# Optimization experiments

Measured on AMD Instinct MI355X. Metric: run time of the kernel, lower is better.

## Reference

```python
import jax, jax.numpy as jnp
import numpy as np

DIM = 192
HEADS = 6
HEAD_DIM = DIM // HEADS
K = 3          # kernel_size
PAD = 1
STRIDE = 2
SCALE = HEAD_DIM ** -0.5
B, H, W = 16, 56, 56


def setup_inputs() -> dict:
    key = jax.random.key(0)
    ks = jax.random.split(key, 6)
    x = jax.random.normal(ks[0], (B, H, W, DIM), jnp.float32)
    # Linear weights stored as [in, out] so y = x @ W + b (== torch x @ W.T)
    Wv = jax.random.normal(ks[1], (DIM, DIM), jnp.float32) * 0.05          # v_pj, no bias
    Wa = jax.random.normal(ks[2], (DIM, K**4 * HEADS), jnp.float32) * 0.05  # attn linear
    ba = jax.random.normal(ks[3], (K**4 * HEADS,), jnp.float32) * 0.01
    Wp = jax.random.normal(ks[4], (DIM, DIM), jnp.float32) * 0.05           # proj
    bp = jax.random.normal(ks[5], (DIM,), jnp.float32) * 0.01
    return {"x": x, "Wv": Wv, "Wa": Wa, "ba": ba, "Wp": Wp, "bp": bp}


def reference(x, Wv, Wa, ba, Wp, bp):
    # Dropout layers act as identity (eval mode).
    Bn, Hn, Wn, C = x.shape
    h = -(-Hn // STRIDE)  # ceil(H/stride) = 28
    w = -(-Wn // STRIDE)
    KK = K * K

    # --- value projection + unfold (im2col over K x K window, stride STRIDE) ---
    v = x @ Wv  # [B,H,W,C]
    vp = jnp.pad(v, ((0, 0), (PAD, PAD), (PAD, PAD), (0, 0)))
    # patches: [B,h,w,K*K,C]; loop is over the fixed 3x3 kernel taps only
    patches = jnp.stack(
        [vp[:, i:i + STRIDE * h:STRIDE, j:j + STRIDE * w:STRIDE, :]
         for i in range(K) for j in range(K)], axis=3)
    patches = patches.reshape(Bn, h * w, KK, HEADS, HEAD_DIM)

    # --- attention weights from avg-pooled map (H divisible by STRIDE here) ---
    pooled = x.reshape(Bn, h, STRIDE, w, STRIDE, C).mean(axis=(2, 4))  # [B,h,w,C]
    a = pooled.reshape(Bn, h * w, C) @ Wa + ba                         # [B,hw,K^4*heads]
    a = a.reshape(Bn, h * w, HEADS, KK, KK) * SCALE
    a = jax.nn.softmax(a, axis=-1)

    # --- windowed attention: [B,hw,heads,K2,K2] x [B,hw,K2,heads,hd] ---
    out = jnp.einsum('bnhpq,bnqhd->bnphd', a, patches)  # [B,hw,K2,heads,hd]
    out = out.reshape(Bn, h, w, KK, C)

    # --- fold (scatter-add of overlapping patches back to HxW) ---
    acc = jnp.zeros((Bn, Hn + 2 * PAD, Wn + 2 * PAD, C), x.dtype)
    idx = 0
    for i in range(K):
        for j in range(K):
            acc = acc.at[:, i:i + STRIDE * h:STRIDE, j:j + STRIDE * w:STRIDE, :].add(out[:, :, :, idx, :])
            idx += 1
    y = acc[:, PAD:PAD + Hn, PAD:PAD + Wn, :]

    return y @ Wp + bp
```

## Files before the change

### kernel.cpp

```cpp
#include <hip/hip_runtime.h>
#include <cstdint>
#include <cstddef>

#define DIMC    192
#define NHEADS  6
#define NATT    486
#define NB      16
#define NH      56
#define NWW     56
#define HPOOL   28
#define WPOOL   28
#define NPIX    784
#define VH      58
#define VW      58
#define MROWS   (NB*NH*NWW)
#define MPOOL   (NB*NPIX)
#define SCALE_A 0.17677669529663687f

using bf16x8 = __attribute__((ext_vector_type(8))) short;
using f32x4  = __attribute__((ext_vector_type(4))) float;

static __device__ __forceinline__ unsigned short f2bf(float f) {
    unsigned int u = __float_as_uint(f);
    unsigned int r = (u + 0x7fffu + ((u >> 16) & 1u)) >> 16;
    return (unsigned short)r;
}
static __device__ __forceinline__ float bf2f(unsigned short u) {
    return __uint_as_float((unsigned int)u << 16);
}

__global__ __launch_bounds__(256)
void prep_kernel(const float* __restrict__ Wv, const float* __restrict__ Wp,
                 const float* __restrict__ Wa,
                 unsigned short* __restrict__ WTv, unsigned short* __restrict__ WTp,
                 unsigned short* __restrict__ WaT, unsigned int* __restrict__ vpu)
{
    int idx = blockIdx.x * 256 + threadIdx.x;
    if (idx < 73728) {
        int sel = idx / 36864;
        int r   = idx - sel * 36864;
        int n   = r / DIMC;
        int k   = r - n * DIMC;
        const float* W = sel ? Wp : Wv;
        unsigned short* WT = sel ? WTp : WTv;
        WT[r] = f2bf(W[k * DIMC + n]);
    } else if (idx < 172032) {
        int r = idx - 73728;
        int n = r / DIMC;
        int k = r - n * DIMC;
        WaT[r] = (n < NATT) ? f2bf(Wa[(size_t)k * NATT + n] * SCALE_A) : (unsigned short)0;
    } else {
        int i2   = idx - 172032;
        int cu   = i2 % 96;
        int rest = i2 / 96;
        int b    = rest / 228;
        int p    = rest - b * 228;
        int hi, wi;
        if (p < 58)       { hi = 0;  wi = p; }
        else if (p < 116) { hi = 57; wi = p - 58; }
        else { int q = p - 116; hi = 1 + (q >> 1); wi = (q & 1) * 57; }
        vpu[(((size_t)b * VH + hi) * VW + wi) * 96 + cu] = 0u;
    }
}

template<int MODE>
__global__ __launch_bounds__(512)
void gemm128_kernel(const void* __restrict__ Av, const unsigned short* __restrict__ WT,
                    const float* __restrict__ bias, void* __restrict__ Cv)
{
    __shared__ unsigned short As[128 * DIMC];

    const int t  = threadIdx.x;
    const int l  = t & 63;
    const int w  = t >> 6;
    const int wr = w >> 1;
    const int wc = w & 1;
    const int by = blockIdx.x;

    if (MODE == 0) {
        const float* Ab = (const float*)Av + (size_t)by * 128 * DIMC;
#pragma unroll
        for (int i = 0; i < 12; ++i) {
            int f = i * 2048 + t * 4;
            float4 v = *(const float4*)(Ab + f);
            int row = f / DIMC;
            int k   = f - row * DIMC;
            ushort4 u;
            u.x = f2bf(v.x); u.y = f2bf(v.y); u.z = f2bf(v.z); u.w = f2bf(v.w);
            int off = (row * 384 + k * 2) ^ ((row & 7) << 4);
            *(ushort4*)((char*)As + off) = u;
        }
    } else {
        const unsigned short* Ab = (const unsigned short*)Av + (size_t)by * 128 * DIMC;
#pragma unroll
        for (int i = 0; i < 6; ++i) {
            int f = i * 4096 + t * 8;
            bf16x8 v = *(const bf16x8*)(Ab + f);
            int row = f / DIMC;
            int k   = f - row * DIMC;
            int off = (row * 384 + k * 2) ^ ((row & 7) << 4);
            *(bf16x8*)((char*)As + off) = v;
        }
    }
    __syncthreads();

    f32x4 acc[2][6];
#pragma unroll
    for (int mi = 0; mi < 2; ++mi)
#pragma unroll
        for (int ni = 0; ni < 6; ++ni) acc[mi][ni] = (f32x4)0.f;

    const int arow0 = wr * 32 + (l & 15);
    const int kb    = (l >> 4) << 4;

#pragma unroll
    for (int ks = 0; ks < 6; ++ks) {
        bf16x8 a[2], b[6];
#pragma unroll
        for (int mi = 0; mi < 2; ++mi) {
            int row = arow0 + mi * 16;
            int off = (row * 384 + ks * 64 + kb) ^ ((row & 7) << 4);
            a[mi] = *(const bf16x8*)((const char*)As + off);
        }
#pragma unroll
        for (int ni = 0; ni < 6; ++ni) {
            int n = wc * 96 + ni * 16 + (l & 15);
            b[ni] = *(const bf16x8*)(WT + (size_t)n * DIMC + ks * 32 + ((l >> 4) << 3));
        }
#pragma unroll
        for (int mi = 0; mi < 2; ++mi)
#pragma unroll
            for (int ni = 0; ni < 6; ++ni)
                acc[mi][ni] = __builtin_amdgcn_mfma_f32_16x16x32_bf16(
                    a[mi], b[ni], acc[mi][ni], 0, 0, 0);
    }

    if (MODE == 0) {
        __syncthreads();
#pragma unroll
        for (int mi = 0; mi < 2; ++mi) {
#pragma unroll
            for (int r = 0; r < 4; ++r) {
                int row = wr * 32 + mi * 16 + ((l >> 4) << 2) + r;
#pragma unroll
                for (int ni = 0; ni < 6; ++ni) {
                    int col = wc * 96 + ni * 16 + (l & 15);
                    As[row * DIMC + col] = f2bf(acc[mi][ni][r]);
                }
            }
        }
        __syncthreads();
#pragma unroll
        for (int i = 0; i < 6; ++i) {
            int f   = i * 4096 + t * 8;
            int row = f / DIMC;
            int k   = f - row * DIMC;
            int m   = by * 128 + row;
            int bb  = m / (NH * NWW);
            int rr  = m - bb * (NH * NWW);
            int hi  = rr / NWW;
            int wi  = rr - hi * NWW;
            bf16x8 v = *(const bf16x8*)&As[f];
            unsigned short* dst = (unsigned short*)Cv +
                (((size_t)bb * VH + hi + 1) * VW + (wi + 1)) * DIMC + k;
            *(bf16x8*)dst = v;
        }
    } else {
        float* fAs = (float*)As;
#pragma unroll
        for (int chunk = 0; chunk < 4; ++chunk) {
            __syncthreads();
            if (wr == chunk) {
#pragma unroll
                for (int mi = 0; mi < 2; ++mi) {
#pragma unroll
                    for (int r = 0; r < 4; ++r) {
                        int rowl = mi * 16 + ((l >> 4) << 2) + r;
#pragma unroll
                        for (int ni = 0; ni < 6; ++ni) {
                            int col = wc * 96 + ni * 16 + (l & 15);
                            fAs[rowl * DIMC + col] = acc[mi][ni][r];
                        }
                    }
                }
            }
            __syncthreads();
#pragma unroll
            for (int i = 0; i < 3; ++i) {
                int f   = i * 2048 + t * 4;
                int row = f / DIMC;
                int k   = f - row * DIMC;
                int m   = by * 128 + chunk * 32 + row;
                float4 v  = *(const float4*)&fAs[f];
                float4 bv = *(const float4*)&bias[k];
                v.x += bv.x; v.y += bv.y; v.z += bv.z; v.w += bv.w;
                *(float4*)((float*)Cv + (size_t)m * DIMC + k) = v;
            }
        }
    }
}

__global__ __launch_bounds__(512)
void pool_attn_mfma_kernel(const float* __restrict__ x, const unsigned short* __restrict__ WaT,
                           const float* __restrict__ ba, unsigned short* __restrict__ attn)
{
    __shared__ unsigned short As[64 * DIMC];
    __shared__ float Cs[16][489];
    __shared__ float ba_s[NATT];

    const int t  = threadIdx.x;
    const int l  = t & 63;
    const int w  = t >> 6;
    const int wr = w >> 2;
    const int wc = w & 3;
    const int by = blockIdx.x;

    if (t < NATT) ba_s[t] = ba[t] * SCALE_A;

#pragma unroll
    for (int i = 0; i < 6; ++i) {
        int f   = i * 2048 + t * 4;
        int row = f / DIMC;
        int k   = f - row * DIMC;
        int m   = by * 64 + row;
        int b   = m / NPIX;
        int r   = m - b * NPIX;
        int hh  = r / WPOOL;
        int ww  = r - hh * WPOOL;
        const float* xp = x + (((size_t)(b * NH + hh * 2)) * NWW + ww * 2) * DIMC + k;
        float4 v0 = *(const float4*)(xp);
        float4 v1 = *(const float4*)(xp + DIMC);
        float4 v2 = *(const float4*)(xp + (size_t)NWW * DIMC);
        float4 v3 = *(const float4*)(xp + (size_t)NWW * DIMC + DIMC);
        ushort4 u;
        u.x = f2bf(0.25f * (v0.x + v1.x + v2.x + v3.x));
        u.y = f2bf(0.25f * (v0.y + v1.y + v2.y + v3.y));
        u.z = f2bf(0.25f * (v0.z + v1.z + v2.z + v3.z));
        u.w = f2bf(0.25f * (v0.w + v1.w + v2.w + v3.w));
        int off = (row * 384 + k * 2) ^ ((row & 7) << 4);
        *(ushort4*)((char*)As + off) = u;
    }
    __syncthreads();

    f32x4 acc[2][8];
#pragma unroll
    for (int mi = 0; mi < 2; ++mi)
#pragma unroll
        for (int ni = 0; ni < 8; ++ni) acc[mi][ni] = (f32x4)0.f;

    const int arow0 = wr * 32 + (l & 15);
    const int kb    = (l >> 4) << 4;

#pragma unroll
    for (int ks = 0; ks < 6; ++ks) {
        bf16x8 a[2], b[8];
#pragma unroll
        for (int mi = 0; mi < 2; ++mi) {
            int row = arow0 + mi * 16;
            int off = (row * 384 + ks * 64 + kb) ^ ((row & 7) << 4);
            a[mi] = *(const bf16x8*)((const char*)As + off);
        }
#pragma unroll
        for (int ni = 0; ni < 8; ++ni) {
            int n = wc * 128 + ni * 16 + (l & 15);
            b[ni] = *(const bf16x8*)(WaT + (size_t)n * DIMC + ks * 32 + ((l >> 4) << 3));
        }
#pragma unroll
        for (int mi = 0; mi < 2; ++mi)
#pragma unroll
            for (int ni = 0; ni < 8; ++ni)
                acc[mi][ni] = __builtin_amdgcn_mfma_f32_16x16x32_bf16(
                    a[mi], b[ni], acc[mi][ni], 0, 0, 0);
    }

#pragma unroll
    for (int r0 = 0; r0 < 64; r0 += 16) {
        const int mi = (r0 >> 4) & 1;
        if (wr == (r0 >> 5)) {
#pragma unroll
            for (int ni = 0; ni < 8; ++ni) {
                int col = wc * 128 + ni * 16 + (l & 15);
                if (col < NATT) {
#pragma unroll
                    for (int r = 0; r < 4; ++r)
                        Cs[((l >> 4) << 2) + r][col] =
                            (mi == 0 ? acc[0][ni][r] : acc[1][ni][r]) + ba_s[col];
                }
            }
        }
        __syncthreads();
        for (int g = t; g < 864; g += 512) {
            int lr = g / 54;
            int cg = g - lr * 54;
            const float* ap = &Cs[lr][cg * 9];
            float mx = ap[0];
#pragma unroll
            for (int q = 1; q < 9; ++q) mx = fmaxf(mx, ap[q]);
            float e[9];
            float sum = 0.f;
#pragma unroll
            for (int q = 0; q < 9; ++q) { e[q] = __expf(ap[q] - mx); sum += e[q]; }
            float inv = 1.f / sum;
            int m = by * 64 + r0 + lr;
            unsigned short* dst = attn + ((size_t)m * 54 + cg) * 16;
#pragma unroll
            for (int q = 0; q < 9; ++q) dst[q] = f2bf(e[q] * inv);
        }
        __syncthreads();
    }
}

template<int NI, int NJ>
static __device__ __forceinline__ void gather_body(
    int b, int p, int qc, int head, int c,
    const unsigned short* __restrict__ attn, const unsigned short* __restrict__ vp,
    unsigned short* __restrict__ y)
{
    const int pr = p >> 1;
    const int qr = qc >> 1;

    float accx = 0.f, accy = 0.f;

#pragma unroll
    for (int wi = 0; wi < NI; ++wi) {
        const bool hv  = (NI == 1) || (wi == 0) || (pr + 1 < HPOOL);
        const int  hhs = hv ? (pr + wi) : (HPOOL - 1);
        const int  iof = (NI == 1) ? 1 : (wi ? 0 : 2);
#pragma unroll
        for (int wj = 0; wj < NJ; ++wj) {
            const bool wv  = (NJ == 1) || (wj == 0) || (qr + 1 < WPOOL);
            const int  wws = wv ? (qr + wj) : (WPOOL - 1);
            const bool ok  = hv && wv;
            const int  jof = (NJ == 1) ? 1 : (wj ? 0 : 2);

            const unsigned short* ap = attn +
                ((size_t)((b * NPIX + hhs * WPOOL + wws) * 54 + head * 9 + iof * 3 + jof)) * 16;
            bf16x8 aw = *(const bf16x8*)ap;
            float a_[9];
#pragma unroll
            for (int k = 0; k < 8; ++k)
                a_[k] = ok ? bf2f((unsigned short)aw[k]) : 0.f;
            a_[8] = ok ? bf2f(ap[8]) : 0.f;

            const unsigned short* vb = vp +
                (((size_t)(b * VH + 2 * hhs)) * VW + 2 * wws) * DIMC + c;
            ushort2 v[9];
#pragma unroll
            for (int qi = 0; qi < 3; ++qi)
#pragma unroll
                for (int qj = 0; qj < 3; ++qj)
                    v[qi * 3 + qj] = *(const ushort2*)(vb + ((size_t)qi * VW + qj) * DIMC);

#pragma unroll
            for (int k = 0; k < 9; ++k) {
                accx = fmaf(a_[k], bf2f(v[k].x), accx);
                accy = fmaf(a_[k], bf2f(v[k].y), accy);
            }
        }
    }
    size_t pix = (size_t)b * (NH * NWW) + (size_t)p * NWW + qc;
    ushort2 r;
    r.x = f2bf(accx);
    r.y = f2bf(accy);
    *(ushort2*)(y + pix * DIMC + c) = r;
}

__global__ __launch_bounds__(192)
void gather_kernel(const unsigned short* __restrict__ attn,
                   const unsigned short* __restrict__ vp,
                   unsigned short* __restrict__ y)
{
    const int t    = threadIdx.x;
    const int pl   = t / 96;
    const int c2   = t - pl * 96;
    const int c    = c2 * 2;
    const int head = c2 >> 4;

    const int flat = blockIdx.x;
    const int wgid = (flat & 7) * 3136 + (flat >> 3);
    const int b    = wgid / 1568;
    const int rr   = wgid - b * 1568;
    const int p    = rr / 28;
    const int wq   = rr - p * 28;
    const int qc   = wq + pl * 28;

    if (p & 1) {
        if (wq & 1) gather_body<2, 2>(b, p, qc, head, c, attn, vp, y);
        else        gather_body<2, 1>(b, p, qc, head, c, attn, vp, y);
    } else {
        if (wq & 1) gather_body<1, 2>(b, p, qc, head, c, attn, vp, y);
        else        gather_body<1, 1>(b, p, qc, head, c, attn, vp, y);
    }
}

extern "C" void kernel_launch(void* const* d_in, const int* in_sizes, int n_in,
                              void* d_out, int out_size, void* d_ws, size_t ws_size,
                              hipStream_t stream)
{
    const float* x  = (const float*)d_in[0];
    const float* Wv = (const float*)d_in[1];
    const float* Wa = (const float*)d_in[2];
    const float* ba = (const float*)d_in[3];
    const float* Wp = (const float*)d_in[4];
    const float* bp = (const float*)d_in[5];
    float* out = (float*)d_out;

    const size_t vp_elems   = (size_t)NB * VH * VW * DIMC;
    const size_t attn_elems = (size_t)MPOOL * 54 * 16;
    const size_t y_elems    = (size_t)MROWS * DIMC;

    unsigned short* vp   = (unsigned short*)d_ws;
    unsigned short* attn = vp + vp_elems;
    unsigned short* y    = attn + attn_elems;
    unsigned short* WTv  = y + y_elems;
    unsigned short* WTp  = WTv + 36864;
    unsigned short* WaT  = WTp + 36864;

    prep_kernel<<<2040, 256, 0, stream>>>(Wv, Wp, Wa, WTv, WTp, WaT, (unsigned int*)vp);

    gemm128_kernel<0><<<MROWS / 128, 512, 0, stream>>>(x, WTv, nullptr, vp);
    pool_attn_mfma_kernel<<<MPOOL / 64, 512, 0, stream>>>(x, WaT, ba, attn);

    gather_kernel<<<25088, 192, 0, stream>>>(attn, vp, y);

    gemm128_kernel<1><<<MROWS / 128, 512, 0, stream>>>(y, WTp, bp, out);
}
```

Measured before the change: 117.2 us.

## Merge value GEMM and pooled attention kernels into one launch; batch gather loads

```diff
diff --git a/kernel.cpp b/kernel.cpp
--- a/kernel.cpp
+++ b/kernel.cpp
@@ -63,44 +63,28 @@
     }
 }
 
-template<int MODE>
-__global__ __launch_bounds__(512)
-void gemm128_kernel(const void* __restrict__ Av, const unsigned short* __restrict__ WT,
-                    const float* __restrict__ bias, void* __restrict__ Cv)
-{
-    __shared__ unsigned short As[128 * DIMC];
-
-    const int t  = threadIdx.x;
+static __device__ __forceinline__
+void gemm0_body(const float* __restrict__ x, const unsigned short* __restrict__ WT,
+                unsigned short* __restrict__ vp, int by, int t, char* smem)
+{
+    unsigned short* As = (unsigned short*)smem;
+
     const int l  = t & 63;
     const int w  = t >> 6;
     const int wr = w >> 1;
     const int wc = w & 1;
-    const int by = blockIdx.x;
-
-    if (MODE == 0) {
-        const float* Ab = (const float*)Av + (size_t)by * 128 * DIMC;
-#pragma unroll
-        for (int i = 0; i < 12; ++i) {
-            int f = i * 2048 + t * 4;
-            float4 v = *(const float4*)(Ab + f);
-            int row = f / DIMC;
-            int k   = f - row * DIMC;
-            ushort4 u;
-            u.x = f2bf(v.x); u.y = f2bf(v.y); u.z = f2bf(v.z); u.w = f2bf(v.w);
-            int off = (row * 384 + k * 2) ^ ((row & 7) << 4);
-            *(ushort4*)((char*)As + off) = u;
-        }
-    } else {
-        const unsigned short* Ab = (const unsigned short*)Av + (size_t)by * 128 * DIMC;
-#pragma unroll
-        for (int i = 0; i < 6; ++i) {
-            int f = i * 4096 + t * 8;
-            bf16x8 v = *(const bf16x8*)(Ab + f);
-            int row = f / DIMC;
-            int k   = f - row * DIMC;
-            int off = (row * 384 + k * 2) ^ ((row & 7) << 4);
-            *(bf16x8*)((char*)As + off) = v;
-        }
+
+    const float* Ab = x + (size_t)by * 128 * DIMC;
+#pragma unroll
+    for (int i = 0; i < 12; ++i) {
+        int f = i * 2048 + t * 4;
+        float4 v = *(const float4*)(Ab + f);
+        int row = f / DIMC;
+        int k   = f - row * DIMC;
+        ushort4 u;
+        u.x = f2bf(v.x); u.y = f2bf(v.y); u.z = f2bf(v.z); u.w = f2bf(v.w);
+        int off = (row * 384 + k * 2) ^ ((row & 7) << 4);
+        *(ushort4*)((char*)As + off) = u;
     }
     __syncthreads();
 
@@ -135,85 +119,49 @@
                     a[mi], b[ni], acc[mi][ni], 0, 0, 0);
     }
 
-    if (MODE == 0) {
-        __syncthreads();
-#pragma unroll
-        for (int mi = 0; mi < 2; ++mi) {
-#pragma unroll
-            for (int r = 0; r < 4; ++r) {
-                int row = wr * 32 + mi * 16 + ((l >> 4) << 2) + r;
-#pragma unroll
-                for (int ni = 0; ni < 6; ++ni) {
-                    int col = wc * 96 + ni * 16 + (l & 15);
-                    As[row * DIMC + col] = f2bf(acc[mi][ni][r]);
-                }
+    __syncthreads();
+#pragma unroll
+    for (int mi = 0; mi < 2; ++mi) {
+#pragma unroll
+        for (int r = 0; r < 4; ++r) {
+            int row = wr * 32 + mi * 16 + ((l >> 4) << 2) + r;
+#pragma unroll
+            for (int ni = 0; ni < 6; ++ni) {
+                int col = wc * 96 + ni * 16 + (l & 15);
+                As[row * DIMC + col] = f2bf(acc[mi][ni][r]);
             }
         }
-        __syncthreads();
-#pragma unroll
-        for (int i = 0; i < 6; ++i) {
-            int f   = i * 4096 + t * 8;
-            int row = f / DIMC;
-            int k   = f - row * DIMC;
-            int m   = by * 128 + row;
-            int bb  = m / (NH * NWW);
-            int rr  = m - bb * (NH * NWW);
-            int hi  = rr / NWW;
-            int wi  = rr - hi * NWW;
-            bf16x8 v = *(const bf16x8*)&As[f];
-            unsigned short* dst = (unsigned short*)Cv +
-                (((size_t)bb * VH + hi + 1) * VW + (wi + 1)) * DIMC + k;
-            *(bf16x8*)dst = v;
-        }
-    } else {
-        float* fAs = (float*)As;
-#pragma unroll
-        for (int chunk = 0; chunk < 4; ++chunk) {
-            __syncthreads();
-            if (wr == chunk) {
-#pragma unroll
-                for (int mi = 0; mi < 2; ++mi) {
-#pragma unroll
-                    for (int r = 0; r < 4; ++r) {
-                        int rowl = mi * 16 + ((l >> 4) << 2) + r;
-#pragma unroll
-                        for (int ni = 0; ni < 6; ++ni) {
-                            int col = wc * 96 + ni * 16 + (l & 15);
-                            fAs[rowl * DIMC + col] = acc[mi][ni][r];
-                        }
-                    }
-                }
-            }
-            __syncthreads();
-#pragma unroll
-            for (int i = 0; i < 3; ++i) {
-                int f   = i * 2048 + t * 4;
-                int row = f / DIMC;
-                int k   = f - row * DIMC;
-                int m   = by * 128 + chunk * 32 + row;
-                float4 v  = *(const float4*)&fAs[f];
-                float4 bv = *(const float4*)&bias[k];
-                v.x += bv.x; v.y += bv.y; v.z += bv.z; v.w += bv.w;
-                *(float4*)((float*)Cv + (size_t)m * DIMC + k) = v;
-            }
-        }
-    }
-}
-
-__global__ __launch_bounds__(512)
-void pool_attn_mfma_kernel(const float* __restrict__ x, const unsigned short* __restrict__ WaT,
-                           const float* __restrict__ ba, unsigned short* __restrict__ attn)
-{
-    __shared__ unsigned short As[64 * DIMC];
-    __shared__ float Cs[16][489];
-    __shared__ float ba_s[NATT];
-
-    const int t  = threadIdx.x;
+    }
+    __syncthreads();
+#pragma unroll
+    for (int i = 0; i < 6; ++i) {
+        int f   = i * 4096 + t * 8;
+        int row = f / DIMC;
+        int k   = f - row * DIMC;
+        int m   = by * 128 + row;
+        int bb  = m / (NH * NWW);
+        int rr  = m - bb * (NH * NWW);
+        int hi  = rr / NWW;
+        int wi  = rr - hi * NWW;
+        bf16x8 v = *(const bf16x8*)&As[f];
+        unsigned short* dst = vp + (((size_t)bb * VH + hi + 1) * VW + (wi + 1)) * DIMC + k;
+        *(bf16x8*)dst = v;
+    }
+}
+
+static __device__ __forceinline__
+void pool_body(const float* __restrict__ x, const unsigned short* __restrict__ WaT,
+               const float* __restrict__ ba, unsigned short* __restrict__ attn,
+               int by, int t, char* smem)
+{
+    unsigned short* As = (unsigned short*)smem;
+    float (*Cs)[489]   = (float(*)[489])(smem + 24576);
+    float* ba_s        = (float*)(smem + 24576 + 31296);
+
     const int l  = t & 63;
     const int w  = t >> 6;
     const int wr = w >> 2;
     const int wc = w & 3;
-    const int by = blockIdx.x;
 
     if (t < NATT) ba_s[t] = ba[t] * SCALE_A;
 
@@ -310,6 +258,106 @@
     }
 }
 
+__global__ __launch_bounds__(512)
+void phase1_kernel(const float* __restrict__ x, const unsigned short* __restrict__ WTv,
+                   const unsigned short* __restrict__ WaT, const float* __restrict__ ba,
+                   unsigned short* __restrict__ vp, unsigned short* __restrict__ attn)
+{
+    __shared__ __align__(16) char smem[57816];
+    const int t = threadIdx.x;
+    if (blockIdx.x < 392) gemm0_body(x, WTv, vp, blockIdx.x, t, smem);
+    else                  pool_body(x, WaT, ba, attn, blockIdx.x - 392, t, smem);
+}
+
+__global__ __launch_bounds__(512)
+void gemm1_kernel(const unsigned short* __restrict__ Av, const unsigned short* __restrict__ WT,
+                  const float* __restrict__ bias, float* __restrict__ Cv)
+{
+    __shared__ unsigned short As[128 * DIMC];
+
+    const int t  = threadIdx.x;
+    const int l  = t & 63;
+    const int w  = t >> 6;
+    const int wr = w >> 1;
+    const int wc = w & 1;
+    const int by = blockIdx.x;
+
+    const unsigned short* Ab = Av + (size_t)by * 128 * DIMC;
+#pragma unroll
+    for (int i = 0; i < 6; ++i) {
+        int f = i * 4096 + t * 8;
+        bf16x8 v = *(const bf16x8*)(Ab + f);
+        int row = f / DIMC;
+        int k   = f - row * DIMC;
+        int off = (row * 384 + k * 2) ^ ((row & 7) << 4);
+        *(bf16x8*)((char*)As + off) = v;
+    }
+    __syncthreads();
+
+    f32x4 acc[2][6];
+#pragma unroll
+    for (int mi = 0; mi < 2; ++mi)
+#pragma unroll
+        for (int ni = 0; ni < 6; ++ni) acc[mi][ni] = (f32x4)0.f;
+
+    const int arow0 = wr * 32 + (l & 15);
+    const int kb    = (l >> 4) << 4;
+
+#pragma unroll
+    for (int ks = 0; ks < 6; ++ks) {
+        bf16x8 a[2], b[6];
+#pragma unroll
+        for (int mi = 0; mi < 2; ++mi) {
+            int row = arow0 + mi * 16;
+            int off = (row * 384 + ks * 64 + kb) ^ ((row & 7) << 4);
+            a[mi] = *(const bf16x8*)((const char*)As + off);
+        }
+#pragma unroll
+        for (int ni = 0; ni < 6; ++ni) {
+            int n = wc * 96 + ni * 16 + (l & 15);
+            b[ni] = *(const bf16x8*)(WT + (size_t)n * DIMC + ks * 32 + ((l >> 4) << 3));
+        }
+#pragma unroll
+        for (int mi = 0; mi < 2; ++mi)
+#pragma unroll
+            for (int ni = 0; ni < 6; ++ni)
+                acc[mi][ni] = __builtin_amdgcn_mfma_f32_16x16x32_bf16(
+                    a[mi], b[ni], acc[mi][ni], 0, 0, 0);
+    }
+
+    float* fAs = (float*)As;
+#pragma unroll
+    for (int chunk = 0; chunk < 4; ++chunk) {
+        __syncthreads();
+        if (wr == chunk) {
+#pragma unroll
+            for (int mi = 0; mi < 2; ++mi) {
+#pragma unroll
+                for (int r = 0; r < 4; ++r) {
+                    int rowl = mi * 16 + ((l >> 4) << 2) + r;
+#pragma unroll
+                    for (int ni = 0; ni < 6; ++ni) {
+                        int col = wc * 96 + ni * 16 + (l & 15);
+                        fAs[rowl * DIMC + col] = acc[mi][ni][r];
+                    }
+                }
+            }
+        }
+        __syncthreads();
+#pragma unroll
+        for (int i = 0; i < 3; ++i) {
+            int f   = i * 2048 + t * 4;
+            int row = f / DIMC;
+            int k   = f - row * DIMC;
+            int m   = by * 128 + chunk * 32 + row;
+            float4 v  = *(const float4*)&fAs[f];
+            float4 bv = *(const float4*)&bias[k];
+            v.x += bv.x; v.y += bv.y; v.z += bv.z; v.w += bv.w;
+            *(float4*)(Cv + (size_t)m * DIMC + k) = v;
+        }
+    }
+}
+
 template<int NI, int NJ>
 static __device__ __forceinline__ void gather_body(
     int b, int p, int qc, int head, int c,
@@ -319,7 +367,10 @@
     const int pr = p >> 1;
     const int qr = qc >> 1;
 
-    float accx = 0.f, accy = 0.f;
+    bf16x8        aw8[NI * NJ];
+    unsigned short aw9[NI * NJ];
+    ushort2       v[NI * NJ][9];
+    bool          ok[NI * NJ];
 
 #pragma unroll
     for (int wi = 0; wi < NI; ++wi) {
@@ -330,34 +381,38 @@
         for (int wj = 0; wj < NJ; ++wj) {
             const bool wv  = (NJ == 1) || (wj == 0) || (qr + 1 < WPOOL);
             const int  wws = wv ? (qr + wj) : (WPOOL - 1);
-            const bool ok  = hv && wv;
             const int  jof = (NJ == 1) ? 1 : (wj ? 0 : 2);
+            const int  idx = wi * NJ + wj;
+            ok[idx] = hv && wv;
 
             const unsigned short* ap = attn +
                 ((size_t)((b * NPIX + hhs * WPOOL + wws) * 54 + head * 9 + iof * 3 + jof)) * 16;
-            bf16x8 aw = *(const bf16x8*)ap;
-            float a_[9];
-#pragma unroll
-            for (int k = 0; k < 8; ++k)
-                a_[k] = ok ? bf2f((unsigned short)aw[k]) : 0.f;
-            a_[8] = ok ? bf2f(ap[8]) : 0.f;
+            aw8[idx] = *(const bf16x8*)ap;
+            aw9[idx] = ap[8];
 
             const unsigned short* vb = vp +
                 (((size_t)(b * VH + 2 * hhs)) * VW + 2 * wws) * DIMC + c;
-            ushort2 v[9];
 #pragma unroll
             for (int qi = 0; qi < 3; ++qi)
 #pragma unroll
                 for (int qj = 0; qj < 3; ++qj)
-                    v[qi * 3 + qj] = *(const ushort2*)(vb + ((size_t)qi * VW + qj) * DIMC);
-
-#pragma unroll
-            for (int k = 0; k < 9; ++k) {
-                accx = fmaf(a_[k], bf2f(v[k].x), accx);
-                accy = fmaf(a_[k], bf2f(v[k].y), accy);
-            }
-        }
-    }
+                    v[idx][qi * 3 + qj] = *(const ushort2*)(vb + ((size_t)qi * VW + qj) * DIMC);
+        }
+    }
+
+    float accx = 0.f, accy = 0.f;
+#pragma unroll
+    for (int idx = 0; idx < NI * NJ; ++idx) {
+#pragma unroll
+        for (int k = 0; k < 9; ++k) {
+            float a = ok[idx]
+                ? ((k < 8) ? bf2f((unsigned short)aw8[idx][k]) : bf2f(aw9[idx]))
+                : 0.f;
+            accx = fmaf(a, bf2f(v[idx][k].x), accx);
+            accy = fmaf(a, bf2f(v[idx][k].y), accy);
+        }
+    }
+
     size_t pix = (size_t)b * (NH * NWW) + (size_t)p * NWW + qc;
     ushort2 r;
     r.x = f2bf(accx);
@@ -418,10 +473,9 @@
 
     prep_kernel<<<2040, 256, 0, stream>>>(Wv, Wp, Wa, WTv, WTp, WaT, (unsigned int*)vp);
 
-    gemm128_kernel<0><<<MROWS / 128, 512, 0, stream>>>(x, WTv, nullptr, vp);
-    pool_attn_mfma_kernel<<<MPOOL / 64, 512, 0, stream>>>(x, WaT, ba, attn);
+    phase1_kernel<<<588, 512, 0, stream>>>(x, WTv, WaT, ba, vp, attn);
 
     gather_kernel<<<25088, 192, 0, stream>>>(attn, vp, y);
 
-    gemm128_kernel<1><<<MROWS / 128, 512, 0, stream>>>(y, WTp, bp, out);
-}
+    gemm1_kernel<<<MROWS / 128, 512, 0, stream>>>(y, WTp, bp, out);
+}
```

Result: faster. 114.0 us (-2.7%).
